# Kernel optimization log

Measured on AMD Instinct MI355X. Metric: run time of the kernel, lower is better.

## Reference

```python
import jax, jax.numpy as jnp
import numpy as np

N_NODES = 100000
N_EDGES = 1600000
IN_C, HID_C, OUT_C = 128, 256, 128


def setup_inputs() -> dict:
    key = jax.random.key(0)
    ks = jax.random.split(key, 6)
    x = jax.random.normal(ks[0], (N_NODES, IN_C), dtype=jnp.float32)
    edge_index = jax.random.randint(ks[1], (2, N_EDGES), 0, N_NODES, dtype=jnp.int64)
    s = 0.05
    W1a = jax.random.normal(ks[2], (IN_C, HID_C), dtype=jnp.float32) * s
    b1a = jnp.zeros((HID_C,), dtype=jnp.float32)
    W2a = jax.random.normal(ks[3], (HID_C, HID_C), dtype=jnp.float32) * s
    b2a = jnp.zeros((HID_C,), dtype=jnp.float32)
    W1b = jax.random.normal(ks[4], (HID_C, HID_C), dtype=jnp.float32) * s
    b1b = jnp.zeros((HID_C,), dtype=jnp.float32)
    W2b = jax.random.normal(ks[5], (HID_C, OUT_C), dtype=jnp.float32) * s
    b2b = jnp.zeros((OUT_C,), dtype=jnp.float32)
    return {"x": x, "edge_index": edge_index, "W1a": W1a, "b1a": b1a,
            "W2a": W2a, "b2a": b2a, "W1b": W1b, "b1b": b1b,
            "W2b": W2b, "b2b": b2b}


def _gin_conv(x, src, dst, W1, b1, W2, b2):
    # GINConv (eps=0): nn( x + sum_{j in N(i)} x_j )
    agg = jax.ops.segment_sum(x[src], dst, num_segments=N_NODES)  # [N, d]
    h = x + agg
    h = jnp.maximum(h @ W1 + b1, 0.0)
    return h @ W2 + b2


def reference(x, edge_index, W1a, b1a, W2a, b2a, W1b, b1b, W2b, b2b):
    src, dst = edge_index[0], edge_index[1]
    h = jnp.maximum(_gin_conv(x, src, dst, W1a, b1a, W2a, b2a), 0.0)  # relu(conv1)
    # dropout is identity in eval mode
    out = _gin_conv(h, src, dst, W1b, b1b, W2b, b2b)  # conv2
    return out
```

## Files before the change

kernel.cpp:

```cpp
#include <hip/hip_runtime.h>


#define N_NODES 100000
#define N_EDGES 1600000

typedef unsigned short ushort_t;
typedef short bf16x8 __attribute__((ext_vector_type(8)));
typedef float floatx4 __attribute__((ext_vector_type(4)));

static __device__ __forceinline__ ushort_t f2bf(float f) {
    unsigned u = __float_as_uint(f);
    u = (u + 0x7FFFu + ((u >> 16) & 1u)) >> 16;
    return (ushort_t)u;
}
static __device__ __forceinline__ unsigned pack2bf(float lo, float hi) {
    return (unsigned)f2bf(lo) | ((unsigned)f2bf(hi) << 16);
}
static __device__ __forceinline__ void addu4(float* acc, const uint4 v) {
    const unsigned w0 = v.x, w1 = v.y, w2 = v.z, w3 = v.w;
    acc[0] += __uint_as_float(w0 << 16);
    acc[1] += __uint_as_float(w0 & 0xFFFF0000u);
    acc[2] += __uint_as_float(w1 << 16);
    acc[3] += __uint_as_float(w1 & 0xFFFF0000u);
    acc[4] += __uint_as_float(w2 << 16);
    acc[5] += __uint_as_float(w2 & 0xFFFF0000u);
    acc[6] += __uint_as_float(w3 << 16);
    acc[7] += __uint_as_float(w3 & 0xFFFF0000u);
}

#define GLOAD_LDS16(g, l)                                                     \
    __builtin_amdgcn_global_load_lds(                                         \
        (const __attribute__((address_space(1))) void*)(g),                   \
        (__attribute__((address_space(3))) void*)(l), 16, 0, 0)

#define NX8 (N_NODES * 128 / 8)
__global__ __launch_bounds__(256) void cvt_fused_kernel(
    const float* __restrict__ X, ushort_t* __restrict__ Xb,
    const float* __restrict__ W1a, const float* __restrict__ W2a,
    const float* __restrict__ W1b, const float* __restrict__ W2b,
    ushort_t* __restrict__ wt1a, ushort_t* __restrict__ wt2a,
    ushort_t* __restrict__ wt1b, ushort_t* __restrict__ wt2b) {
    int i = blockIdx.x * 256 + threadIdx.x;
    if (i < NX8) {
        const float4 a = ((const float4*)X)[2 * i];
        const float4 b = ((const float4*)X)[2 * i + 1];
        uint4 r;
        r.x = pack2bf(a.x, a.y);
        r.y = pack2bf(a.z, a.w);
        r.z = pack2bf(b.x, b.y);
        r.w = pack2bf(b.z, b.w);
        ((uint4*)Xb)[i] = r;
        return;
    }
    i -= NX8;
    if (i < 32768) {
        int k = i >> 8, n = i & 255;
        wt1a[n * 128 + k] = f2bf(W1a[i]);
    } else if (i < 98304) {
        int j = i - 32768, k = j >> 8, n = j & 255;
        wt2a[n * 256 + k] = f2bf(W2a[j]);
    } else if (i < 163840) {
        int j = i - 98304, k = j >> 8, n = j & 255;
        wt1b[n * 256 + k] = f2bf(W1b[j]);
    } else if (i < 196608) {
        int j = i - 163840, k = j >> 7, n = j & 127;
        wt2b[n * 256 + k] = f2bf(W2b[j]);
    }
}

__global__ __launch_bounds__(256) void hist_kernel(const int* __restrict__ src,
                                                   const int* __restrict__ dst,
                                                   int* __restrict__ deg, int nE) {
    for (int e = blockIdx.x * 256 + threadIdx.x; e < nE; e += gridDim.x * 256) {
        int d = dst[e];
        int s = src[e];
        if ((unsigned)d < (unsigned)N_NODES && (unsigned)s < (unsigned)N_NODES)
            atomicAdd(&deg[d], 1);
    }
}

__global__ __launch_bounds__(256) void fill_kernel(const int* __restrict__ src,
                                                   const int* __restrict__ dst,
                                                   int* __restrict__ cursor,
                                                   int* __restrict__ csr_src, int nE) {
    for (int e = blockIdx.x * 256 + threadIdx.x; e < nE; e += gridDim.x * 256) {
        int d = dst[e];
        int s = src[e];
        if ((unsigned)d < (unsigned)N_NODES && (unsigned)s < (unsigned)N_NODES) {
            int pos = atomicAdd(&cursor[d], 1);
            csr_src[pos] = s;
        }
    }
}

__global__ __launch_bounds__(256) void scan1_kernel(const int* __restrict__ deg,
                                                    int* __restrict__ bsum, int n) {
    __shared__ int l[256];
    int b = blockIdx.x, t = threadIdx.x;
    int base = b * 1024 + t * 4;
    int s = 0;
#pragma unroll
    for (int k = 0; k < 4; ++k) {
        int i = base + k;
        if (i < n) s += deg[i];
    }
    l[t] = s;
    __syncthreads();
    for (int off = 128; off > 0; off >>= 1) {
        if (t < off) l[t] += l[t + off];
        __syncthreads();
    }
    if (t == 0) bsum[b] = l[0];
}

__global__ __launch_bounds__(128) void scan2_kernel(const int* __restrict__ bsum,
                                                    int* __restrict__ boff, int nb) {
    __shared__ int l[128];
    int t = threadIdx.x;
    int v = (t < nb) ? bsum[t] : 0;
    l[t] = v;
    __syncthreads();
    for (int off = 1; off < 128; off <<= 1) {
        int add = (t >= off) ? l[t - off] : 0;
        __syncthreads();
        l[t] += add;
        __syncthreads();
    }
    if (t < nb) boff[t] = l[t] - v;
}

__global__ __launch_bounds__(256) void scan3_kernel(const int* __restrict__ deg,
                                                    const int* __restrict__ boff,
                                                    int* __restrict__ row_ptr,
                                                    int* __restrict__ cursor, int n) {
    __shared__ int l[256];
    int b = blockIdx.x, t = threadIdx.x;
    int base = b * 1024 + t * 4;
    int d[4];
    int s = 0;
#pragma unroll
    for (int k = 0; k < 4; ++k) {
        int i = base + k;
        d[k] = (i < n) ? deg[i] : 0;
        s += d[k];
    }
    l[t] = s;
    __syncthreads();
    for (int off = 1; off < 256; off <<= 1) {
        int add = (t >= off) ? l[t - off] : 0;
        __syncthreads();
        l[t] += add;
        __syncthreads();
    }
    int run = boff[b] + l[t] - s;
#pragma unroll
    for (int k = 0; k < 4; ++k) {
        int i = base + k;
        if (i < n) {
            row_ptr[i] = run;
            cursor[i] = run;
        }
        run += d[k];
    }
}

template <int C, int U>
__global__ __launch_bounds__(256) void agg_gather_kernel(
    const ushort_t* __restrict__ X, ushort_t* __restrict__ T,
    const int* __restrict__ row_ptr, const int* __restrict__ deg,
    const int* __restrict__ csr_src, const ushort_t* __restrict__ zrow, int nN) {
    constexpr int G = C / 8;
    constexpr int NPW = 64 / G;
    constexpr int B = U * NPW;
    const int lane = threadIdx.x & 63;
    const int wid = threadIdx.x >> 6;
    const int node = blockIdx.x * 4 + wid;
    if (node >= nN) return;
    const int sub = lane / G;
    const int coff = (lane % G) * 8;

    float acc[8];
#pragma unroll
    for (int k = 0; k < 8; ++k) acc[k] = 0.f;

    const int base = row_ptr[node];
    const int dg = deg[node];
    for (int j0 = 0; j0 < dg; j0 += 64) {
        int cnt = dg - j0;
        if (cnt > 64) cnt = 64;
        int nidx = (lane < cnt) ? csr_src[base + j0 + lane] : 0;
        if ((unsigned)nidx >= (unsigned)N_NODES) nidx = 0;
        for (int j = 0; j < cnt; j += B) {
            uint4 v[U];
#pragma unroll
            for (int u = 0; u < U; ++u) {
                int jj = j + u * NPW + sub;
                bool ok = jj < cnt;
                int idx = __shfl(nidx, ok ? jj : 0);
                const ushort_t* p = ok ? (X + (size_t)idx * C) : zrow;
                v[u] = *(const uint4*)(p + coff);
            }
#pragma unroll
            for (int u = 0; u < U; ++u) addu4(acc, v[u]);
        }
    }
    if (sub == 0) {
        uint4 v = *(const uint4*)(X + (size_t)node * C + coff);
        addu4(acc, v);
    }
#pragma unroll
    for (int off = G; off < 64; off <<= 1)
#pragma unroll
        for (int k = 0; k < 8; ++k) acc[k] += __shfl_xor(acc[k], off);

    if (lane < G) {
        uint4 r;
        r.x = pack2bf(acc[0], acc[1]);
        r.y = pack2bf(acc[2], acc[3]);
        r.z = pack2bf(acc[4], acc[5]);
        r.w = pack2bf(acc[6], acc[7]);
        *(uint4*)(T + (size_t)node * C + coff) = r;
    }
}

template <int K1, int N2, bool RELU2, typename OT>
__global__ __launch_bounds__(256, 3) void mlp_kernel(
    const ushort_t* __restrict__ A, const ushort_t* __restrict__ Wt1,
    const float* __restrict__ b1, const ushort_t* __restrict__ Wt2,
    const float* __restrict__ b2, OT* __restrict__ C, int M) {
    constexpr int N1 = 256, BM = 64, BK = 32;
    constexpr int NPW2 = N2 / 4;
    constexpr int RN2 = NPW2 / 16;
    __shared__ ushort_t As[BM * BK];
    __shared__ ushort_t Bs[N1 * BK];
    __shared__ ushort_t U[BM * N1];

    const int lane = threadIdx.x & 63;
    const int wid = threadIdx.x >> 6;
    const int l15 = lane & 15;
    const int q = lane >> 4;
    const int srow = lane >> 2;
    const int scol = (lane & 3) * 8;
    const int bm = blockIdx.x * BM;

    floatx4 acc[4][4];
#pragma unroll
    for (int mi = 0; mi < 4; ++mi)
#pragma unroll
        for (int ni = 0; ni < 4; ++ni) {
            floatx4 z = {0.f, 0.f, 0.f, 0.f};
            acc[mi][ni] = z;
        }

    for (int kt = 0; kt < K1; kt += BK) {
        {
            const int gr = bm + wid * 16 + srow;
            if (gr < M)
                GLOAD_LDS16(A + (size_t)gr * K1 + kt + scol, &As[(wid * 16) * BK]);
        }
#pragma unroll
        for (int u = 0; u < 4; ++u) {
            const int row = wid * 64 + u * 16;
            GLOAD_LDS16(Wt1 + (size_t)(row + srow) * K1 + kt + scol, &Bs[row * BK]);
        }
        __syncthreads();
        bf16x8 av[4], bv[4];
#pragma unroll
        for (int mi = 0; mi < 4; ++mi)
            av[mi] = *(const bf16x8*)&Bs[(wid * 64 + mi * 16 + l15) * BK + q * 8];
#pragma unroll
        for (int ni = 0; ni < 4; ++ni)
            bv[ni] = *(const bf16x8*)&As[(ni * 16 + l15) * BK + q * 8];
#pragma unroll
        for (int mi = 0; mi < 4; ++mi)
#pragma unroll
            for (int ni = 0; ni < 4; ++ni)
                acc[mi][ni] = __builtin_amdgcn_mfma_f32_16x16x32_bf16(
                    av[mi], bv[ni], acc[mi][ni], 0, 0, 0);
        __syncthreads();
    }

#pragma unroll
    for (int mi = 0; mi < 4; ++mi) {
        const int h0 = wid * 64 + mi * 16 + q * 4;
        const float4 b4 = *(const float4*)&b1[h0];
#pragma unroll
        for (int ni = 0; ni < 4; ++ni) {
            const int node = ni * 16 + l15;
            float v0 = acc[mi][ni][0] + b4.x; v0 = v0 > 0.f ? v0 : 0.f;
            float v1 = acc[mi][ni][1] + b4.y; v1 = v1 > 0.f ? v1 : 0.f;
            float v2 = acc[mi][ni][2] + b4.z; v2 = v2 > 0.f ? v2 : 0.f;
            float v3 = acc[mi][ni][3] + b4.w; v3 = v3 > 0.f ? v3 : 0.f;
            uint2 w;
            w.x = pack2bf(v0, v1);
            w.y = pack2bf(v2, v3);
            int byte = node * (N1 * 2) + h0 * 2;
            byte ^= (node & 7) << 4;
            *(uint2*)((char*)U + byte) = w;
        }
    }
    __syncthreads();

#pragma unroll
    for (int mi = 0; mi < 4; ++mi)
#pragma unroll
        for (int ni = 0; ni < 4; ++ni) {
            floatx4 z = {0.f, 0.f, 0.f, 0.f};
            acc[mi][ni] = z;
        }

    for (int kt = 0; kt < N1; kt += BK) {
#pragma unroll
        for (int u = 0; u < RN2; ++u) {
            const int row = wid * NPW2 + u * 16;
            GLOAD_LDS16(Wt2 + (size_t)(row + srow) * N1 + kt + scol, &Bs[row * BK]);
        }
        __syncthreads();
        bf16x8 av[4], bv[RN2];
#pragma unroll
        for (int mi = 0; mi < 4; ++mi) {
            const int node = mi * 16 + l15;
            const int byte =
                (node * (N1 * 2) + kt * 2 + q * 16) ^ ((node & 7) << 4);
            av[mi] = *(const bf16x8*)((const char*)U + byte);
        }
#pragma unroll
        for (int ni = 0; ni < RN2; ++ni)
            bv[ni] = *(const bf16x8*)&Bs[(wid * NPW2 + ni * 16 + l15) * BK + q * 8];
#pragma unroll
        for (int mi = 0; mi < 4; ++mi)
#pragma unroll
            for (int ni = 0; ni < RN2; ++ni)
                acc[mi][ni] = __builtin_amdgcn_mfma_f32_16x16x32_bf16(
                    av[mi], bv[ni], acc[mi][ni], 0, 0, 0);
        __syncthreads();
    }

    float bval[RN2];
#pragma unroll
    for (int ni = 0; ni < RN2; ++ni) bval[ni] = b2[wid * NPW2 + ni * 16 + l15];
#pragma unroll
    for (int mi = 0; mi < 4; ++mi) {
#pragma unroll
        for (int r = 0; r < 4; ++r) {
            const int row = bm + mi * 16 + q * 4 + r;
            if (row < M) {
#pragma unroll
                for (int ni = 0; ni < RN2; ++ni) {
                    const int col = wid * NPW2 + ni * 16 + l15;
                    float v = acc[mi][ni][r] + bval[ni];
                    if (RELU2) v = v > 0.f ? v : 0.f;
                    if constexpr (sizeof(OT) == 2)
                        C[(size_t)row * N2 + col] = f2bf(v);
                    else
                        C[(size_t)row * N2 + col] = v;
                }
            }
        }
    }
}

extern "C" void kernel_launch(void* const* d_in, const int* in_sizes, int n_in,
                              void* d_out, int out_size, void* d_ws, size_t ws_size,
                              hipStream_t stream) {
    const float* x   = (const float*)d_in[0];
    const int*   ei  = (const int*)d_in[1];
    const float* W1a = (const float*)d_in[2];
    const float* b1a = (const float*)d_in[3];
    const float* W2a = (const float*)d_in[4];
    const float* b2a = (const float*)d_in[5];
    const float* W1b = (const float*)d_in[6];
    const float* b1b = (const float*)d_in[7];
    const float* W2b = (const float*)d_in[8];
    const float* b2b = (const float*)d_in[9];
    const int* src = ei;
    const int* dst = ei + N_EDGES;
    float* out = (float*)d_out;

    char* base = (char*)d_ws;
    size_t o = 0;
    ushort_t* wt1a = (ushort_t*)(base + o); o += 128 * 256 * 2;
    ushort_t* wt2a = (ushort_t*)(base + o); o += 256 * 256 * 2;
    ushort_t* wt1b = (ushort_t*)(base + o); o += 256 * 256 * 2;
    ushort_t* wt2b = (ushort_t*)(base + o); o += 256 * 128 * 2;
    o = (o + 255) & ~(size_t)255;
    ushort_t* zrow = (ushort_t*)(base + o); o += 512;
    int* deg     = (int*)(base + o); o += (size_t)N_NODES * 4;
    int* row_ptr = (int*)(base + o); o += (size_t)N_NODES * 4;
    int* cursor  = (int*)(base + o); o += (size_t)N_NODES * 4;
    int* bsum    = (int*)(base + o); o += 128 * 4;
    int* boff    = (int*)(base + o); o += 128 * 4;
    o = (o + 255) & ~(size_t)255;
    int* csr_src = (int*)(base + o); o += (size_t)N_EDGES * 4;
    o = (o + 255) & ~(size_t)255;
    ushort_t* t1   = (ushort_t*)(base + o); o += (size_t)N_NODES * 128 * 2;
    ushort_t* tbig = (ushort_t*)(base + o); o += (size_t)N_NODES * 256 * 2;
    o += 128 * 1024;
    (void)ws_size; (void)o; (void)in_sizes; (void)n_in; (void)out_size;

    ushort_t* inter = (ushort_t*)d_out;
    ushort_t* xb    = (ushort_t*)d_out;

    cvt_fused_kernel<<<(NX8 + 196608 + 255) / 256, 256, 0, stream>>>(
        x, xb, W1a, W2a, W1b, W2b, wt1a, wt2a, wt1b, wt2b);

    const int NB = (N_NODES + 1023) / 1024;
    hipMemsetAsync(zrow, 0, 512 + (size_t)N_NODES * 4, stream);
    hist_kernel<<<2048, 256, 0, stream>>>(src, dst, deg, N_EDGES);
    scan1_kernel<<<NB, 256, 0, stream>>>(deg, bsum, N_NODES);
    scan2_kernel<<<1, 128, 0, stream>>>(bsum, boff, NB);
    scan3_kernel<<<NB, 256, 0, stream>>>(deg, boff, row_ptr, cursor, N_NODES);
    fill_kernel<<<2048, 256, 0, stream>>>(src, dst, cursor, csr_src, N_EDGES);

    const int ga = (N_NODES + 3) / 4;
    const int gf = (N_NODES + 63) / 64;

    agg_gather_kernel<128, 4><<<ga, 256, 0, stream>>>(xb, t1, row_ptr, deg,
                                                      csr_src, zrow, N_NODES);
    mlp_kernel<128, 256, true, ushort_t><<<gf, 256, 0, stream>>>(
        t1, wt1a, b1a, wt2a, b2a, inter, N_NODES);

    agg_gather_kernel<256, 8><<<ga, 256, 0, stream>>>(inter, tbig, row_ptr,
                                                      deg, csr_src, zrow, N_NODES);
    mlp_kernel<256, 128, false, float><<<gf, 256, 0, stream>>>(
        tbig, wt1b, b1b, wt2b, b2b, out, N_NODES);
}
```

Measured before the change: 594.0 us.

## Partition edges into destination buckets before CSR fill for locality

Result: faster. 557.7 us (-6.1%).

```diff
diff --git a/kernel.cpp b/kernel.cpp
--- a/kernel.cpp
+++ b/kernel.cpp
@@ -3,6 +3,8 @@
 
 #define N_NODES 100000
 #define N_EDGES 1600000
+#define NBUCK 13
+#define PCAP 200000
 
 typedef unsigned short ushort_t;
 typedef short bf16x8 __attribute__((ext_vector_type(8)));
@@ -68,28 +70,50 @@
     }
 }
 
-__global__ __launch_bounds__(256) void hist_kernel(const int* __restrict__ src,
-                                                   const int* __restrict__ dst,
-                                                   int* __restrict__ deg, int nE) {
-    for (int e = blockIdx.x * 256 + threadIdx.x; e < nE; e += gridDim.x * 256) {
-        int d = dst[e];
-        int s = src[e];
-        if ((unsigned)d < (unsigned)N_NODES && (unsigned)s < (unsigned)N_NODES)
-            atomicAdd(&deg[d], 1);
-    }
-}
-
-__global__ __launch_bounds__(256) void fill_kernel(const int* __restrict__ src,
-                                                   const int* __restrict__ dst,
-                                                   int* __restrict__ cursor,
-                                                   int* __restrict__ csr_src, int nE) {
-    for (int e = blockIdx.x * 256 + threadIdx.x; e < nE; e += gridDim.x * 256) {
-        int d = dst[e];
-        int s = src[e];
-        if ((unsigned)d < (unsigned)N_NODES && (unsigned)s < (unsigned)N_NODES) {
-            int pos = atomicAdd(&cursor[d], 1);
-            csr_src[pos] = s;
-        }
+__global__ __launch_bounds__(256) void part_kernel(
+    const int* __restrict__ src, const int* __restrict__ dst,
+    int* __restrict__ deg, int* __restrict__ pcur,
+    uint2* __restrict__ ebuf, int nE) {
+    __shared__ int cnt[NBUCK];
+    __shared__ int gbase[NBUCK];
+    for (int e0 = blockIdx.x * 256; e0 < nE; e0 += gridDim.x * 256) {
+        const int e = e0 + threadIdx.x;
+        if (threadIdx.x < NBUCK) cnt[threadIdx.x] = 0;
+        __syncthreads();
+        int s = 0, d = 0, b = 0, mypos = 0;
+        bool ok = false;
+        if (e < nE) {
+            d = dst[e];
+            s = src[e];
+            ok = (unsigned)d < (unsigned)N_NODES && (unsigned)s < (unsigned)N_NODES;
+            if (ok) {
+                b = d >> 13;
+                atomicAdd(&deg[d], 1);
+                mypos = atomicAdd(&cnt[b], 1);
+            }
+        }
+        __syncthreads();
+        if (threadIdx.x < NBUCK)
+            gbase[threadIdx.x] = atomicAdd(&pcur[threadIdx.x], cnt[threadIdx.x]);
+        __syncthreads();
+        if (ok) {
+            int p = gbase[b] + mypos;
+            if (p < PCAP) ebuf[(size_t)b * PCAP + p] = make_uint2((unsigned)s, (unsigned)d);
+        }
+    }
+}
+
+__global__ __launch_bounds__(256) void bfill_kernel(
+    const uint2* __restrict__ ebuf, const int* __restrict__ pcur,
+    int* __restrict__ cursor, int* __restrict__ csr_src) {
+    const int b = blockIdx.y;
+    int n = pcur[b];
+    if (n > PCAP) n = PCAP;
+    const uint2* eb = ebuf + (size_t)b * PCAP;
+    for (int i = blockIdx.x * 256 + threadIdx.x; i < n; i += gridDim.x * 256) {
+        const uint2 sd = eb[i];
+        int pos = atomicAdd(&cursor[(int)sd.y], 1);
+        csr_src[pos] = (int)sd.x;
     }
 }
 
@@ -386,6 +410,7 @@
     o = (o + 255) & ~(size_t)255;
     ushort_t* zrow = (ushort_t*)(base + o); o += 512;
     int* deg     = (int*)(base + o); o += (size_t)N_NODES * 4;
+    int* pcur    = (int*)(base + o); o += 64;
     int* row_ptr = (int*)(base + o); o += (size_t)N_NODES * 4;
     int* cursor  = (int*)(base + o); o += (size_t)N_NODES * 4;
     int* bsum    = (int*)(base + o); o += 128 * 4;
@@ -396,6 +421,7 @@
     ushort_t* t1   = (ushort_t*)(base + o); o += (size_t)N_NODES * 128 * 2;
     ushort_t* tbig = (ushort_t*)(base + o); o += (size_t)N_NODES * 256 * 2;
     o += 128 * 1024;
+    uint2* ebuf = (uint2*)t1;
     (void)ws_size; (void)o; (void)in_sizes; (void)n_in; (void)out_size;
 
     ushort_t* inter = (ushort_t*)d_out;
@@ -405,12 +431,12 @@
         x, xb, W1a, W2a, W1b, W2b, wt1a, wt2a, wt1b, wt2b);
 
     const int NB = (N_NODES + 1023) / 1024;
-    hipMemsetAsync(zrow, 0, 512 + (size_t)N_NODES * 4, stream);
-    hist_kernel<<<2048, 256, 0, stream>>>(src, dst, deg, N_EDGES);
+    hipMemsetAsync(zrow, 0, 512 + (size_t)N_NODES * 4 + 64, stream);
+    part_kernel<<<2048, 256, 0, stream>>>(src, dst, deg, pcur, ebuf, N_EDGES);
     scan1_kernel<<<NB, 256, 0, stream>>>(deg, bsum, N_NODES);
     scan2_kernel<<<1, 128, 0, stream>>>(bsum, boff, NB);
     scan3_kernel<<<NB, 256, 0, stream>>>(deg, boff, row_ptr, cursor, N_NODES);
-    fill_kernel<<<2048, 256, 0, stream>>>(src, dst, cursor, csr_src, N_EDGES);
+    bfill_kernel<<<dim3(1024, NBUCK), 256, 0, stream>>>(ebuf, pcur, cursor, csr_src);
 
     const int ga = (N_NODES + 3) / 4;
     const int gf = (N_NODES + 63) / 64;
```

## Fuse degree histogram into convert kernel and bucket CSR fill by destination

Applied to the files above, without the earlier changes.

New measurement: 542.7 us. 1.09x faster.

```diff
diff --git a/kernel.cpp b/kernel.cpp
--- a/kernel.cpp
+++ b/kernel.cpp
@@ -3,6 +3,7 @@
 
 #define N_NODES 100000
 #define N_EDGES 1600000
+#define NBUCK 13
 
 typedef unsigned short ushort_t;
 typedef short bf16x8 __attribute__((ext_vector_type(8)));
@@ -34,12 +35,16 @@
         (__attribute__((address_space(3))) void*)(l), 16, 0, 0)
 
 #define NX8 (N_NODES * 128 / 8)
+#define CVT_TOTAL (NX8 + 196608)
+#define HIST_THREADS (2048 * 256)
 __global__ __launch_bounds__(256) void cvt_fused_kernel(
     const float* __restrict__ X, ushort_t* __restrict__ Xb,
     const float* __restrict__ W1a, const float* __restrict__ W2a,
     const float* __restrict__ W1b, const float* __restrict__ W2b,
     ushort_t* __restrict__ wt1a, ushort_t* __restrict__ wt2a,
-    ushort_t* __restrict__ wt1b, ushort_t* __restrict__ wt2b) {
+    ushort_t* __restrict__ wt1b, ushort_t* __restrict__ wt2b,
+    const int* __restrict__ src, const int* __restrict__ dst,
+    int* __restrict__ deg, int nE) {
     int i = blockIdx.x * 256 + threadIdx.x;
     if (i < NX8) {
         const float4 a = ((const float4*)X)[2 * i];
@@ -52,26 +57,24 @@
         ((uint4*)Xb)[i] = r;
         return;
     }
-    i -= NX8;
-    if (i < 32768) {
-        int k = i >> 8, n = i & 255;
-        wt1a[n * 128 + k] = f2bf(W1a[i]);
-    } else if (i < 98304) {
-        int j = i - 32768, k = j >> 8, n = j & 255;
-        wt2a[n * 256 + k] = f2bf(W2a[j]);
-    } else if (i < 163840) {
-        int j = i - 98304, k = j >> 8, n = j & 255;
-        wt1b[n * 256 + k] = f2bf(W1b[j]);
-    } else if (i < 196608) {
-        int j = i - 163840, k = j >> 7, n = j & 127;
-        wt2b[n * 256 + k] = f2bf(W2b[j]);
-    }
-}
-
-__global__ __launch_bounds__(256) void hist_kernel(const int* __restrict__ src,
-                                                   const int* __restrict__ dst,
-                                                   int* __restrict__ deg, int nE) {
-    for (int e = blockIdx.x * 256 + threadIdx.x; e < nE; e += gridDim.x * 256) {
+    if (i < CVT_TOTAL) {
+        i -= NX8;
+        if (i < 32768) {
+            int k = i >> 8, n = i & 255;
+            wt1a[n * 128 + k] = f2bf(W1a[i]);
+        } else if (i < 98304) {
+            int j = i - 32768, k = j >> 8, n = j & 255;
+            wt2a[n * 256 + k] = f2bf(W2a[j]);
+        } else if (i < 163840) {
+            int j = i - 98304, k = j >> 8, n = j & 255;
+            wt1b[n * 256 + k] = f2bf(W1b[j]);
+        } else {
+            int j = i - 163840, k = j >> 7, n = j & 127;
+            wt2b[n * 256 + k] = f2bf(W2b[j]);
+        }
+        return;
+    }
+    for (int e = i - CVT_TOTAL; e < nE; e += HIST_THREADS) {
         int d = dst[e];
         int s = src[e];
         if ((unsigned)d < (unsigned)N_NODES && (unsigned)s < (unsigned)N_NODES)
@@ -83,12 +86,22 @@
                                                    const int* __restrict__ dst,
                                                    int* __restrict__ cursor,
                                                    int* __restrict__ csr_src, int nE) {
-    for (int e = blockIdx.x * 256 + threadIdx.x; e < nE; e += gridDim.x * 256) {
-        int d = dst[e];
-        int s = src[e];
-        if ((unsigned)d < (unsigned)N_NODES && (unsigned)s < (unsigned)N_NODES) {
-            int pos = atomicAdd(&cursor[d], 1);
-            csr_src[pos] = s;
+    for (int e0 = blockIdx.x * 256; e0 < nE; e0 += gridDim.x * 256) {
+        const int e = e0 + threadIdx.x;
+        int s = 0, d = -1;
+        if (e < nE) {
+            d = dst[e];
+            s = src[e];
+            if (!((unsigned)d < (unsigned)N_NODES && (unsigned)s < (unsigned)N_NODES))
+                d = -1;
+        }
+        const int b = (d >= 0) ? (d >> 13) : -1;
+        for (int bk = 0; bk < NBUCK; ++bk) {
+            if (b == bk) {
+                int pos = atomicAdd(&cursor[d], 1);
+                csr_src[pos] = s;
+            }
+            __syncthreads();
         }
     }
 }
@@ -401,12 +414,12 @@
     ushort_t* inter = (ushort_t*)d_out;
     ushort_t* xb    = (ushort_t*)d_out;
 
-    cvt_fused_kernel<<<(NX8 + 196608 + 255) / 256, 256, 0, stream>>>(
-        x, xb, W1a, W2a, W1b, W2b, wt1a, wt2a, wt1b, wt2b);
+    hipMemsetAsync(zrow, 0, 512 + (size_t)N_NODES * 4, stream);
+
+    cvt_fused_kernel<<<CVT_TOTAL / 256 + 2048, 256, 0, stream>>>(
+        x, xb, W1a, W2a, W1b, W2b, wt1a, wt2a, wt1b, wt2b, src, dst, deg, N_EDGES);
 
     const int NB = (N_NODES + 1023) / 1024;
-    hipMemsetAsync(zrow, 0, 512 + (size_t)N_NODES * 4, stream);
-    hist_kernel<<<2048, 256, 0, stream>>>(src, dst, deg, N_EDGES);
     scan1_kernel<<<NB, 256, 0, stream>>>(deg, bsum, N_NODES);
     scan2_kernel<<<1, 128, 0, stream>>>(bsum, boff, NB);
     scan3_kernel<<<NB, 256, 0, stream>>>(deg, boff, row_ptr, cursor, N_NODES);
```
